# Kernel optimization log

Measured on AMD Instinct MI355X. Metric: run time of the kernel, lower is better.

The kernel has to match this reference:

```python
import jax, jax.numpy as jnp
import numpy as np

N = 100000
IN_DIM = 256
OUT_DIM = 256
E = 3200000
SLOPE = 0.2


def setup_inputs() -> dict:
    key = jax.random.key(0)
    ks = jax.random.split(key, 14)
    xav = lambda k, shape: jax.random.normal(k, shape, jnp.float32) * np.sqrt(2.0 / sum(shape))
    inp = {
        "H": jax.random.normal(ks[0], (N, IN_DIM), jnp.float32),
        "W0": xav(ks[1], (IN_DIM, OUT_DIM)),
        "W1": xav(ks[2], (IN_DIM, OUT_DIM)),
        "W2": xav(ks[3], (IN_DIM, OUT_DIM)),
        "a0": xav(ks[4], (2 * OUT_DIM,)),
        "a1": xav(ks[5], (2 * OUT_DIM,)),
        "a2": xav(ks[6], (2 * OUT_DIM,)),
        "bias": jnp.zeros((OUT_DIM,), jnp.float32),
    }
    for i, r in enumerate(["0", "1", "2"]):
        inp["row" + r] = jax.random.randint(ks[7 + 2 * i], (E,), 0, N, jnp.int32)
        inp["col" + r] = jax.random.randint(ks[8 + 2 * i], (E,), 0, N, jnp.int32)
    return inp


def _gat_type(H, W, a, row, col):
    # Wh: [N, out_dim]
    Wh = H @ W
    # attention logits per edge: leaky_relu(a_dst . Wh[row] + a_src . Wh[col])
    s_dst = Wh @ a[:OUT_DIM]   # [N]
    s_src = Wh @ a[OUT_DIM:]   # [N]
    e = jax.nn.leaky_relu(s_dst[row] + s_src[col], SLOPE)  # [E]
    # segment softmax over destination node (row)
    e_max = jax.ops.segment_max(e, row, num_segments=N)    # [N]
    e_shifted = jnp.exp(e - e_max[row])
    e_sum = jax.ops.segment_sum(e_shifted, row, num_segments=N)
    alpha = e_shifted / jnp.maximum(e_sum[row], 1e-12)     # [E]
    # weighted aggregation of source features into destinations
    return jax.ops.segment_sum(alpha[:, None] * Wh[col], row, num_segments=N)


def reference(H, row0, col0, row1, col1, row2, col2, W0, W1, W2, a0, a1, a2, bias):
    out = _gat_type(H, W0, a0, row0, col0)
    out = out + _gat_type(H, W1, a1, row1, col1)
    out = out + _gat_type(H, W2, a2, row2, col2)
    return out + bias
```

## Files before the change

### kernel.cpp

```cpp
#include <hip/hip_runtime.h>
#include <cstdint>
#include <cstddef>

#define DIM 256
#define SLOPE 0.2f
#define BSHIFT 8
#define SLOTS 9216
#define TILE 4096

typedef __attribute__((ext_vector_type(8))) short short8;
typedef __attribute__((ext_vector_type(4))) float f32x4;

__device__ __forceinline__ unsigned short f2bf(float f) {
  unsigned u = __float_as_uint(f);
  u += 0x7fffu + ((u >> 16) & 1u);
  return (unsigned short)(u >> 16);
}
__device__ __forceinline__ float bf2f(unsigned short h) {
  return __uint_as_float(((unsigned)h) << 16);
}


__device__ __forceinline__ void bin_edges_body(
    int bx, int ty, int* hist, int* curs, const int* __restrict__ rr,
    const int* __restrict__ cc, int* __restrict__ bcnt, unsigned* __restrict__ pairs,
    int E, int NB) {
  const int t = threadIdx.x;
  const int base = bx * TILE;
  for (int i = t; i < NB; i += 256) hist[i] = 0;
  __syncthreads();
  int rows[TILE / 256];
#pragma unroll
  for (int i = 0; i < TILE / 256; ++i) {
    int e = base + t + i * 256;
    int r = (e < E) ? rr[e] : -1;
    rows[i] = r;
    if (r >= 0) atomicAdd(&hist[r >> BSHIFT], 1);
  }
  __syncthreads();
  for (int b = t; b < NB; b += 256) {
    int h = hist[b];
    int off = h ? atomicAdd(&bcnt[ty * NB + b], h) : 0;
    curs[b] = b * SLOTS + off;
  }
  __syncthreads();
  unsigned* pt = pairs + (size_t)ty * NB * SLOTS;
#pragma unroll
  for (int i = 0; i < TILE / 256; ++i) {
    int e = base + t + i * 256;
    if (e >= E) continue;
    int r = rows[i];
    int b = r >> BSHIFT;
    int pos = atomicAdd(&curs[b], 1);
    if (pos - b * SLOTS < SLOTS)
      pt[pos] = ((unsigned)(r & 255) << 17) | (unsigned)cc[e];
  }
}

__device__ __forceinline__ void bsort_body(
    int b, int ty, char* smem, const int* __restrict__ bcnt,
    unsigned* __restrict__ pairs, int* __restrict__ rp, int* __restrict__ deg,
    int N, int NB) {
  int* hist = (int*)smem;
  int* excl = hist + 256;
  int* curs = excl + 256;
  unsigned* stage = (unsigned*)(curs + 256);
  const int t = threadIdx.x;
  int cnt = bcnt[ty * NB + b];
  if (cnt > SLOTS) cnt = SLOTS;
  unsigned* pb = pairs + (size_t)ty * NB * SLOTS + (size_t)b * SLOTS;
  hist[t] = 0;
  __syncthreads();
  for (int i = t; i < cnt; i += 256) atomicAdd(&hist[pb[i] >> 17], 1);
  __syncthreads();
  int v = hist[t];
  excl[t] = v;
  __syncthreads();
  for (int off = 1; off < 256; off <<= 1) {
    int u = (t >= off) ? excl[t - off] : 0;
    __syncthreads();
    excl[t] += u;
    __syncthreads();
  }
  int ex = excl[t] - v;
  curs[t] = ex;
  int r = (b << BSHIFT) + t;
  if (r < N) {
    rp[(size_t)ty * N + r] = b * SLOTS + ex;
    deg[(size_t)ty * N + r] = v;
  }
  __syncthreads();
  for (int i = t; i < cnt; i += 256) {
    unsigned p = pb[i];
    int pos = atomicAdd(&curs[p >> 17], 1);
    stage[pos] = p;
  }
  __syncthreads();
  for (int i = t; i < cnt; i += 256) pb[i] = stage[i];
}

__device__ __forceinline__ void gemm3_body(
    int bx, char* smem, const float* __restrict__ H, const unsigned short* __restrict__ Wt,
    const float* __restrict__ a0, const float* __restrict__ a1,
    const float* __restrict__ a2, unsigned short* __restrict__ Whb,
    float* __restrict__ s_dst, float* __restrict__ s_src, int N, size_t wstride) {
  unsigned short(*Hs)[264] = (unsigned short(*)[264])smem;
  unsigned short(*Os)[4][264] = (unsigned short(*)[4][264])(smem + 128 * 264 * 2);
  const int t = threadIdx.x;
  const int r0 = bx * 128;
#pragma unroll
  for (int i = 0; i < 32; ++i) {
    int idx = t + i * 256;
    int row = idx >> 6;
    int c4 = idx & 63;
    int r = r0 + row;
    float4 h = (r < N) ? *(const float4*)&H[(size_t)r * DIM + c4 * 4]
                       : make_float4(0.f, 0.f, 0.f, 0.f);
    unsigned lo = (unsigned)f2bf(h.x) | ((unsigned)f2bf(h.y) << 16);
    unsigned hi = (unsigned)f2bf(h.z) | ((unsigned)f2bf(h.w) << 16);
    *(uint2*)&Hs[row][c4 * 4] = make_uint2(lo, hi);
  }
  __syncthreads();
  const int wave = t >> 6, lane = t & 63;
  const int q = lane >> 4, m = lane & 15;
  const int rowbase = wave * 32;
  short8 Af0[8], Af1[8];
#pragma unroll
  for (int k0 = 0; k0 < 8; ++k0) {
    Af0[k0] = *(const short8*)&Hs[rowbase + m][k0 * 32 + q * 8];
    Af1[k0] = *(const short8*)&Hs[rowbase + 16 + m][k0 * 32 + q * 8];
  }
  const float* aptr[3] = {a0, a1, a2};
  for (int ty = 0; ty < 3; ++ty) {
    const unsigned short* Wtt = Wt + (size_t)ty * DIM * DIM;
    const float* a = aptr[ty];
    f32x4 acc0[16], acc1[16];
#pragma unroll
    for (int j = 0; j < 16; ++j) {
      acc0[j] = (f32x4){0.f, 0.f, 0.f, 0.f};
      acc1[j] = (f32x4){0.f, 0.f, 0.f, 0.f};
    }
#pragma unroll
    for (int k0 = 0; k0 < 8; ++k0) {
#pragma unroll
      for (int j = 0; j < 16; ++j) {
        short8 Bf = *(const short8*)&Wtt[(size_t)(j * 16 + m) * DIM + k0 * 32 + q * 8];
        acc0[j] = __builtin_amdgcn_mfma_f32_16x16x32_bf16(Af0[k0], Bf, acc0[j], 0, 0, 0);
        acc1[j] = __builtin_amdgcn_mfma_f32_16x16x32_bf16(Af1[k0], Bf, acc1[j], 0, 0, 0);
      }
    }
    float pd0[4] = {0, 0, 0, 0}, ps0[4] = {0, 0, 0, 0};
    float pd1[4] = {0, 0, 0, 0}, ps1[4] = {0, 0, 0, 0};
#pragma unroll
    for (int j = 0; j < 16; ++j) {
      int col = j * 16 + m;
      float ad = a[col], as = a[DIM + col];
#pragma unroll
      for (int reg = 0; reg < 4; ++reg) {
        float v0 = acc0[j][reg], v1 = acc1[j][reg];
        pd0[reg] += v0 * ad;
        ps0[reg] += v0 * as;
        pd1[reg] += v1 * ad;
        ps1[reg] += v1 * as;
      }
    }
#pragma unroll
    for (int off = 8; off >= 1; off >>= 1) {
#pragma unroll
      for (int reg = 0; reg < 4; ++reg) {
        pd0[reg] += __shfl_down(pd0[reg], off);
        ps0[reg] += __shfl_down(ps0[reg], off);
        pd1[reg] += __shfl_down(pd1[reg], off);
        ps1[reg] += __shfl_down(ps1[reg], off);
      }
    }
    if (m == 0) {
#pragma unroll
      for (int reg = 0; reg < 4; ++reg) {
        int ra = r0 + rowbase + q * 4 + reg;
        int rb = ra + 16;
        if (ra < N) {
          s_dst[(size_t)ty * N + ra] = pd0[reg];
          s_src[(size_t)ty * N + ra] = ps0[reg];
        }
        if (rb < N) {
          s_dst[(size_t)ty * N + rb] = pd1[reg];
          s_src[(size_t)ty * N + rb] = ps1[reg];
        }
      }
    }
    unsigned short* wout = Whb + (size_t)ty * wstride;
#pragma unroll
    for (int g = 0; g < 2; ++g) {
#pragma unroll
      for (int p = 0; p < 4; ++p) {
        if (q == p) {
#pragma unroll
          for (int j = 0; j < 16; ++j)
#pragma unroll
            for (int reg = 0; reg < 4; ++reg)
              Os[wave][reg][j * 16 + m] = f2bf(g ? acc1[j][reg] : acc0[j][reg]);
        }
#pragma unroll
        for (int rr = 0; rr < 4; ++rr) {
          int r = r0 + rowbase + g * 16 + p * 4 + rr;
          if (r < N)
            *(uint2*)&wout[(size_t)r * DIM + lane * 4] =
                *(const uint2*)&Os[wave][rr][lane * 4];
        }
      }
    }
  }
}


__global__ __launch_bounds__(256) void prep_kernel(
    const float* __restrict__ W0, const float* __restrict__ W1,
    const float* __restrict__ W2, unsigned short* __restrict__ Wt,
    const int* __restrict__ r0, const int* __restrict__ r1, const int* __restrict__ r2,
    const int* __restrict__ c0, const int* __restrict__ c1, const int* __restrict__ c2,
    int* __restrict__ bcnt, unsigned* __restrict__ pairs, int E, int NB, int eb) {
  __shared__ int smem[1024];
  const int bx = blockIdx.x;
  if (bx < 768) {
    int ty = bx >> 8, k = bx & 255, n = threadIdx.x;
    const float* W = ty == 0 ? W0 : (ty == 1 ? W1 : W2);
    Wt[((size_t)ty * DIM + n) * DIM + k] = f2bf(W[k * DIM + n]);
    return;
  }
  int e2 = bx - 768;
  int ty = e2 / eb, bxx = e2 % eb;
  const int* rr = ty == 0 ? r0 : (ty == 1 ? r1 : r2);
  const int* cc = ty == 0 ? c0 : (ty == 1 ? c1 : c2);
  bin_edges_body(bxx, ty, smem, smem + 512, rr, cc, bcnt, pairs, E, NB);
}

__global__ __launch_bounds__(256, 2) void compute_kernel(
    const float* __restrict__ H, const unsigned short* __restrict__ Wt,
    const float* __restrict__ a0, const float* __restrict__ a1,
    const float* __restrict__ a2, unsigned short* __restrict__ Whb,
    float* __restrict__ s_dst, float* __restrict__ s_src, int N, size_t wstride,
    const int* __restrict__ bcnt, unsigned* __restrict__ pairs,
    int* __restrict__ rp, int* __restrict__ deg, int NB, int gemm_blocks) {
  __shared__ __align__(16) char smem[76032];
  const int bx = blockIdx.x;
  if (bx < gemm_blocks) {
    gemm3_body(bx, smem, H, Wt, a0, a1, a2, Whb, s_dst, s_src, N, wstride);
  } else {
    int e = bx - gemm_blocks;
    bsort_body(e % NB, e / NB, smem, bcnt, pairs, rp, deg, N, NB);
  }
}

__global__ __launch_bounds__(256) void bucket_sort_kernel(
    const int* __restrict__ bcnt, unsigned* __restrict__ pairs,
    int* __restrict__ rp, int* __restrict__ deg, int N, int NB) {
  __shared__ __align__(16) char smem[39936];
  bsort_body(blockIdx.x, blockIdx.y, smem, bcnt, pairs, rp, deg, N, NB);
}

__global__ __launch_bounds__(256, 2) void gemm_scores_kernel(
    const float* __restrict__ H, const unsigned short* __restrict__ Wt,
    const float* __restrict__ a, unsigned short* __restrict__ Whb,
    float* __restrict__ s_dst, float* __restrict__ s_src, int N) {
  __shared__ unsigned short Hs[64][264];
  __shared__ unsigned short Os[4][16][264];
  const int t = threadIdx.x;
  const int r0 = blockIdx.x * 64;
#pragma unroll
  for (int i = 0; i < 16; ++i) {
    int idx = t + i * 256;
    int row = idx >> 6;
    int c4 = idx & 63;
    int r = r0 + row;
    float4 h = (r < N) ? *(const float4*)&H[(size_t)r * DIM + c4 * 4]
                       : make_float4(0.f, 0.f, 0.f, 0.f);
    unsigned lo = (unsigned)f2bf(h.x) | ((unsigned)f2bf(h.y) << 16);
    unsigned hi = (unsigned)f2bf(h.z) | ((unsigned)f2bf(h.w) << 16);
    *(uint2*)&Hs[row][c4 * 4] = make_uint2(lo, hi);
  }
  __syncthreads();
  const int wave = t >> 6, lane = t & 63;
  const int q = lane >> 4, m = lane & 15;
  const int rowbase = wave * 16;
  short8 Af[8];
#pragma unroll
  for (int k0 = 0; k0 < 8; ++k0)
    Af[k0] = *(const short8*)&Hs[rowbase + m][k0 * 32 + q * 8];
  f32x4 acc[16];
#pragma unroll
  for (int j = 0; j < 16; ++j) acc[j] = (f32x4){0.f, 0.f, 0.f, 0.f};
#pragma unroll
  for (int k0 = 0; k0 < 8; ++k0) {
#pragma unroll
    for (int j = 0; j < 16; ++j) {
      short8 Bf = *(const short8*)&Wt[(size_t)(j * 16 + m) * DIM + k0 * 32 + q * 8];
      acc[j] = __builtin_amdgcn_mfma_f32_16x16x32_bf16(Af[k0], Bf, acc[j], 0, 0, 0);
    }
  }
  float pd[4] = {0, 0, 0, 0}, ps[4] = {0, 0, 0, 0};
#pragma unroll
  for (int j = 0; j < 16; ++j) {
    int col = j * 16 + m;
    float ad = a[col], as = a[DIM + col];
#pragma unroll
    for (int reg = 0; reg < 4; ++reg) {
      float v = acc[j][reg];
      pd[reg] += v * ad;
      ps[reg] += v * as;
      Os[wave][q * 4 + reg][col] = f2bf(v);
    }
  }
#pragma unroll
  for (int off = 8; off >= 1; off >>= 1) {
#pragma unroll
    for (int reg = 0; reg < 4; ++reg) {
      pd[reg] += __shfl_down(pd[reg], off);
      ps[reg] += __shfl_down(ps[reg], off);
    }
  }
  if (m == 0) {
#pragma unroll
    for (int reg = 0; reg < 4; ++reg) {
      int r = r0 + rowbase + q * 4 + reg;
      if (r < N) {
        s_dst[r] = pd[reg];
        s_src[r] = ps[reg];
      }
    }
  }
  __syncthreads();
#pragma unroll
  for (int row = 0; row < 16; ++row) {
    int r = r0 + rowbase + row;
    if (r < N)
      *(uint2*)&Whb[(size_t)r * DIM + lane * 4] = *(const uint2*)&Os[wave][row][lane * 4];
  }
}

__global__ __launch_bounds__(256) void gat_fused_kernel(
    const int* __restrict__ rp, const int* __restrict__ deg,
    const unsigned* __restrict__ pairs,
    const float* __restrict__ s_dst, const float* __restrict__ s_src,
    const unsigned short* __restrict__ Whb,
    const float* __restrict__ bias, float* __restrict__ out, int N, int NB,
    size_t wstride) {
  __shared__ uint2 ebuf[4][64];
  int n = (int)((blockIdx.x * (unsigned)blockDim.x + threadIdx.x) >> 6);
  if (n >= N) return;
  const int wid = (threadIdx.x >> 6);
  const int lane = threadIdx.x & 63;
  float4 total = {0.f, 0.f, 0.f, 0.f};
  for (int t = 0; t < 3; ++t) {
    int beg = rp[(size_t)t * N + n], d = deg[(size_t)t * N + n];
    if (d == 0) continue;
    int end = beg + d;
    const unsigned* pcol = pairs + (size_t)t * NB * SLOTS;
    const float* ss = s_src + (size_t)t * N;
    float sd = s_dst[(size_t)t * N + n];
    const unsigned short* wbase = Whb + (size_t)t * wstride + lane * 4;
    float mx = -__builtin_inff();
    for (int p = beg + lane; p < end; p += 64) {
      float v = sd + ss[pcol[p] & 0x1FFFFu];
      v = v > 0.f ? v : SLOPE * v;
      mx = fmaxf(mx, v);
    }
#pragma unroll
    for (int off = 32; off >= 1; off >>= 1) mx = fmaxf(mx, __shfl_down(mx, off));
    mx = __shfl(mx, 0);
    float4 acc = {0.f, 0.f, 0.f, 0.f};
    float psum = 0.f;
    for (int base = beg; base < end; base += 64) {
      int myp = base + lane;
      int cnt = end - base;
      if (cnt > 64) cnt = 64;
      unsigned myc = 0;
      float mype = 0.f;
      if (myp < end) {
        myc = pcol[myp] & 0x1FFFFu;
        float v = sd + ss[myc];
        v = v > 0.f ? v : SLOPE * v;
        mype = __expf(v - mx);
      }
      psum += mype;
      ebuf[wid][lane] = make_uint2(myc, __float_as_uint(mype));
#pragma unroll 8
      for (int j = 0; j < cnt; ++j) {
        uint2 cp = ebuf[wid][j];
        float pe = __uint_as_float(cp.y);
        ushort4 w = *(const ushort4*)&wbase[(size_t)cp.x * DIM];
        acc.x += pe * bf2f(w.x);
        acc.y += pe * bf2f(w.y);
        acc.z += pe * bf2f(w.z);
        acc.w += pe * bf2f(w.w);
      }
    }
#pragma unroll
    for (int off = 32; off >= 1; off >>= 1) psum += __shfl_down(psum, off);
    psum = __shfl(psum, 0);
    float inv = 1.f / fmaxf(psum, 1e-12f);
    total.x += acc.x * inv;
    total.y += acc.y * inv;
    total.z += acc.z * inv;
    total.w += acc.w * inv;
  }
  float4 cur = ((const float4*)bias)[lane];
  cur.x += total.x;
  cur.y += total.y;
  cur.z += total.z;
  cur.w += total.w;
  *((float4*)(out + (size_t)n * DIM) + lane) = cur;
}

__global__ __launch_bounds__(256) void gat_node_kernel(
    const int* __restrict__ rp, const int* __restrict__ deg,
    const unsigned* __restrict__ pcol,
    const float* __restrict__ s_dst, const float* __restrict__ s_src,
    const unsigned short* __restrict__ Whb,
    const float* __restrict__ bias, float* __restrict__ out, int N, int first) {
  __shared__ uint2 ebuf[4][64];
  int n = (int)((blockIdx.x * (unsigned)blockDim.x + threadIdx.x) >> 6);
  if (n >= N) return;
  const int wid = (threadIdx.x >> 6);
  const int lane = threadIdx.x & 63;
  int beg = rp[n], d = deg[n], end = beg + d;
  if (!first && d == 0) return;
  float sd = s_dst[n];
  float mx = -__builtin_inff();
  for (int p = beg + lane; p < end; p += 64) {
    float v = sd + s_src[pcol[p] & 0x1FFFFu];
    v = v > 0.f ? v : SLOPE * v;
    mx = fmaxf(mx, v);
  }
#pragma unroll
  for (int off = 32; off >= 1; off >>= 1) mx = fmaxf(mx, __shfl_down(mx, off));
  mx = __shfl(mx, 0);
  const unsigned short* wbase = Whb + lane * 4;
  float4 acc = {0.f, 0.f, 0.f, 0.f};
  float psum = 0.f;
  for (int base = beg; base < end; base += 64) {
    int myp = base + lane;
    int cnt = end - base;
    if (cnt > 64) cnt = 64;
    unsigned myc = 0;
    float mype = 0.f;
    if (myp < end) {
      myc = pcol[myp] & 0x1FFFFu;
      float v = sd + s_src[myc];
      v = v > 0.f ? v : SLOPE * v;
      mype = __expf(v - mx);
    }
    psum += mype;
    ebuf[wid][lane] = make_uint2(myc, __float_as_uint(mype));
#pragma unroll 8
    for (int j = 0; j < cnt; ++j) {
      uint2 cp = ebuf[wid][j];
      float pe = __uint_as_float(cp.y);
      ushort4 w = *(const ushort4*)&wbase[(size_t)cp.x * DIM];
      acc.x += pe * bf2f(w.x);
      acc.y += pe * bf2f(w.y);
      acc.z += pe * bf2f(w.z);
      acc.w += pe * bf2f(w.w);
    }
  }
#pragma unroll
  for (int off = 32; off >= 1; off >>= 1) psum += __shfl_down(psum, off);
  psum = __shfl(psum, 0);
  float inv = 1.f / fmaxf(psum, 1e-12f);
  float4* o = (float4*)(out + (size_t)n * DIM) + lane;
  float4 cur = first ? ((const float4*)bias)[lane] : *o;
  cur.x += acc.x * inv;
  cur.y += acc.y * inv;
  cur.z += acc.z * inv;
  cur.w += acc.w * inv;
  *o = cur;
}

static inline size_t align256(size_t x) { return (x + 255) & ~(size_t)255; }

extern "C" void kernel_launch(void* const* d_in, const int* in_sizes, int n_in,
                              void* d_out, int out_size, void* d_ws, size_t ws_size,
                              hipStream_t stream) {
  const float* H = (const float*)d_in[0];
  const float* W[3] = {(const float*)d_in[1], (const float*)d_in[2], (const float*)d_in[3]};
  const float* a[3] = {(const float*)d_in[4], (const float*)d_in[5], (const float*)d_in[6]};
  const float* bias = (const float*)d_in[7];
  const int* row[3] = {(const int*)d_in[8], (const int*)d_in[10], (const int*)d_in[12]};
  const int* col[3] = {(const int*)d_in[9], (const int*)d_in[11], (const int*)d_in[13]};
  const int N = in_sizes[0] / DIM;
  const int E = in_sizes[8];
  const int NB = (N + 255) >> BSHIFT;
  float* out = (float*)d_out;

  char* ws = (char*)d_ws;
  size_t off = 0;
  unsigned short* Wt = (unsigned short*)(ws + off);
  off = align256(off + (size_t)3 * DIM * DIM * sizeof(unsigned short));
  float* s_dst = (float*)(ws + off);
  off = align256(off + (size_t)3 * N * sizeof(float));
  float* s_src = (float*)(ws + off);
  off = align256(off + (size_t)3 * N * sizeof(float));
  int* bcnt = (int*)(ws + off);
  off = align256(off + (size_t)3 * NB * sizeof(int));
  int* rp = (int*)(ws + off);
  off = align256(off + (size_t)3 * N * sizeof(int));
  int* deg = (int*)(ws + off);
  off = align256(off + (size_t)3 * N * sizeof(int));
  unsigned* pairs = (unsigned*)(ws + off);
  off = align256(off + (size_t)3 * NB * SLOTS * sizeof(unsigned));
  unsigned short* Whb = (unsigned short*)(ws + off);
  const size_t whb_bytes = align256((size_t)N * DIM * sizeof(unsigned short));
  const size_t wstride = whb_bytes / sizeof(unsigned short);
  const int fused = (ws_size >= off + 3 * whb_bytes) ? 1 : 0;

  const int eb = (E + TILE - 1) / TILE;
  hipMemsetAsync(bcnt, 0, (size_t)3 * NB * sizeof(int), stream);
  prep_kernel<<<768 + 3 * eb, 256, 0, stream>>>(W[0], W[1], W[2], Wt, row[0], row[1], row[2],
                                                col[0], col[1], col[2], bcnt, pairs, E, NB, eb);

  const int gat_blocks = (N * 64 + 255) / 256;
  if (fused) {
    const int gemm_blocks = (N + 127) / 128;
    compute_kernel<<<gemm_blocks + 3 * NB, 256, 0, stream>>>(
        H, Wt, a[0], a[1], a[2], Whb, s_dst, s_src, N, wstride, bcnt, pairs, rp, deg, NB,
        gemm_blocks);
    gat_fused_kernel<<<gat_blocks, 256, 0, stream>>>(rp, deg, pairs, s_dst, s_src, Whb, bias,
                                                     out, N, NB, wstride);
  } else {
    bucket_sort_kernel<<<dim3(NB, 3), 256, 0, stream>>>(bcnt, pairs, rp, deg, N, NB);
    for (int t = 0; t < 3; ++t) {
      gemm_scores_kernel<<<(N + 63) / 64, 256, 0, stream>>>(H, Wt + (size_t)t * DIM * DIM,
                                                            a[t], Whb, s_dst + (size_t)t * N,
                                                            s_src + (size_t)t * N, N);
      gat_node_kernel<<<gat_blocks, 256, 0, stream>>>(
          rp + (size_t)t * N, deg + (size_t)t * N, pairs + (size_t)t * NB * SLOTS,
          s_dst + (size_t)t * N, s_src + (size_t)t * N, Whb, bias, out, N, t == 0 ? 1 : 0);
    }
  }
  (void)n_in;
  (void)out_size;
  (void)ws_size;
}
```

Baseline: 1.387 ms.

## Overlap type-0 aggregation with type-1/2 GEMMs in an interleaved kernel

The fused compute kernel now runs only the type-0 GEMM alongside the bucket sort. A new kernel interleaves blocks that run a leaner GEMM for types 1 and 2 with blocks that aggregate type-0 edges and write bias plus the type-0 result. A final kernel then adds the type-1 and type-2 aggregations into the output with a read-modify-write. This is meant to hide GEMM compute behind memory-bound gather work, at the cost of an extra pass over the output and relying on blocks being scheduled in index order.

```diff
diff --git a/kernel.cpp b/kernel.cpp
--- a/kernel.cpp
+++ b/kernel.cpp
@@ -103,7 +103,8 @@
     int bx, char* smem, const float* __restrict__ H, const unsigned short* __restrict__ Wt,
     const float* __restrict__ a0, const float* __restrict__ a1,
     const float* __restrict__ a2, unsigned short* __restrict__ Whb,
-    float* __restrict__ s_dst, float* __restrict__ s_src, int N, size_t wstride) {
+    float* __restrict__ s_dst, float* __restrict__ s_src, int N, size_t wstride,
+    int tycount) {
   unsigned short(*Hs)[264] = (unsigned short(*)[264])smem;
   unsigned short(*Os)[4][264] = (unsigned short(*)[4][264])(smem + 128 * 264 * 2);
   const int t = threadIdx.x;
@@ -131,7 +132,7 @@
     Af1[k0] = *(const short8*)&Hs[rowbase + 16 + m][k0 * 32 + q * 8];
   }
   const float* aptr[3] = {a0, a1, a2};
-  for (int ty = 0; ty < 3; ++ty) {
+  for (int ty = 0; ty < tycount; ++ty) {
     const unsigned short* Wtt = Wt + (size_t)ty * DIM * DIM;
     const float* a = aptr[ty];
     f32x4 acc0[16], acc1[16];
@@ -208,6 +209,98 @@
             *(uint2*)&wout[(size_t)r * DIM + lane * 4] =
                 *(const uint2*)&Os[wave][rr][lane * 4];
         }
+      }
+    }
+  }
+}
+
+__device__ __forceinline__ void gemm1_lean_body(
+    int bx, int ty, char* smem, const float* __restrict__ H,
+    const unsigned short* __restrict__ Wt, const float* __restrict__ a,
+    unsigned short* __restrict__ Whb, float* __restrict__ s_dst,
+    float* __restrict__ s_src, int N, size_t wstride) {
+  unsigned short(*Os)[4][264] = (unsigned short(*)[4][264])smem;
+  const int t = threadIdx.x;
+  const int r0 = bx * 64;
+  const int wave = t >> 6, lane = t & 63;
+  const int q = lane >> 4, m = lane & 15;
+  const int rowbase = wave * 16;
+  const int myrow = r0 + rowbase + m;
+  short8 Af[8];
+#pragma unroll
+  for (int k0 = 0; k0 < 8; ++k0) {
+    short8 v = (short8){0, 0, 0, 0, 0, 0, 0, 0};
+    if (myrow < N) {
+      const float* hp = &H[(size_t)myrow * DIM + k0 * 32 + q * 8];
+      float4 x = *(const float4*)hp;
+      float4 y = *(const float4*)(hp + 4);
+      v[0] = (short)f2bf(x.x); v[1] = (short)f2bf(x.y);
+      v[2] = (short)f2bf(x.z); v[3] = (short)f2bf(x.w);
+      v[4] = (short)f2bf(y.x); v[5] = (short)f2bf(y.y);
+      v[6] = (short)f2bf(y.z); v[7] = (short)f2bf(y.w);
+    }
+    Af[k0] = v;
+  }
+  const unsigned short* Wtt = Wt + (size_t)ty * DIM * DIM;
+  unsigned short* wout = Whb + (size_t)ty * wstride;
+  float pd[4] = {0, 0, 0, 0}, ps[4] = {0, 0, 0, 0};
+  for (int jh = 0; jh < 2; ++jh) {
+    f32x4 acc[8];
+#pragma unroll
+    for (int j = 0; j < 8; ++j) acc[j] = (f32x4){0.f, 0.f, 0.f, 0.f};
+#pragma unroll
+    for (int k0 = 0; k0 < 8; ++k0) {
+#pragma unroll
+      for (int j = 0; j < 8; ++j) {
+        int col16 = jh * 8 + j;
+        short8 Bf = *(const short8*)&Wtt[(size_t)(col16 * 16 + m) * DIM + k0 * 32 + q * 8];
+        acc[j] = __builtin_amdgcn_mfma_f32_16x16x32_bf16(Af[k0], Bf, acc[j], 0, 0, 0);
+      }
+    }
+#pragma unroll
+    for (int j = 0; j < 8; ++j) {
+      int col = (jh * 8 + j) * 16 + m;
+      float ad = a[col], as = a[DIM + col];
+#pragma unroll
+      for (int reg = 0; reg < 4; ++reg) {
+        float v = acc[j][reg];
+        pd[reg] += v * ad;
+        ps[reg] += v * as;
+      }
+    }
+#pragma unroll
+    for (int p = 0; p < 4; ++p) {
+      if (q == p) {
+#pragma unroll
+        for (int j = 0; j < 8; ++j)
+#pragma unroll
+          for (int reg = 0; reg < 4; ++reg)
+            Os[wave][reg][(jh * 8 + j) * 16 + m] = f2bf(acc[j][reg]);
+      }
+#pragma unroll
+      for (int rr = 0; rr < 4; ++rr) {
+        int r = r0 + rowbase + p * 4 + rr;
+        if (r < N)
+          *(unsigned*)&wout[(size_t)r * DIM + jh * 128 + lane * 2] =
+              *(const unsigned*)&Os[wave][rr][jh * 128 + lane * 2];
+      }
+    }
+  }
+#pragma unroll
+  for (int off = 8; off >= 1; off >>= 1) {
+#pragma unroll
+    for (int reg = 0; reg < 4; ++reg) {
+      pd[reg] += __shfl_down(pd[reg], off);
+      ps[reg] += __shfl_down(ps[reg], off);
+    }
+  }
+  if (m == 0) {
+#pragma unroll
+    for (int reg = 0; reg < 4; ++reg) {
+      int r = r0 + rowbase + q * 4 + reg;
+      if (r < N) {
+        s_dst[(size_t)ty * N + r] = pd[reg];
+        s_src[(size_t)ty * N + r] = ps[reg];
       }
     }
   }
@@ -241,109 +334,96 @@
     const float* __restrict__ a2, unsigned short* __restrict__ Whb,
     float* __restrict__ s_dst, float* __restrict__ s_src, int N, size_t wstride,
     const int* __restrict__ bcnt, unsigned* __restrict__ pairs,
-    int* __restrict__ rp, int* __restrict__ deg, int NB, int gemm_blocks) {
+    int* __restrict__ rp, int* __restrict__ deg, int NB, int gemm_blocks,
+    int tycount) {
   __shared__ __align__(16) char smem[76032];
   const int bx = blockIdx.x;
   if (bx < gemm_blocks) {
-    gemm3_body(bx, smem, H, Wt, a0, a1, a2, Whb, s_dst, s_src, N, wstride);
+    gemm3_body(bx, smem, H, Wt, a0, a1, a2, Whb, s_dst, s_src, N, wstride, tycount);
   } else {
     int e = bx - gemm_blocks;
     bsort_body(e % NB, e / NB, smem, bcnt, pairs, rp, deg, N, NB);
   }
 }
 
-__global__ __launch_bounds__(256) void bucket_sort_kernel(
-    const int* __restrict__ bcnt, unsigned* __restrict__ pairs,
-    int* __restrict__ rp, int* __restrict__ deg, int N, int NB) {
-  __shared__ __align__(16) char smem[39936];
-  bsort_body(blockIdx.x, blockIdx.y, smem, bcnt, pairs, rp, deg, N, NB);
-}
-
-__global__ __launch_bounds__(256, 2) void gemm_scores_kernel(
+__global__ __launch_bounds__(256, 4) void gat0_gemm_kernel(
     const float* __restrict__ H, const unsigned short* __restrict__ Wt,
-    const float* __restrict__ a, unsigned short* __restrict__ Whb,
-    float* __restrict__ s_dst, float* __restrict__ s_src, int N) {
-  __shared__ unsigned short Hs[64][264];
-  __shared__ unsigned short Os[4][16][264];
-  const int t = threadIdx.x;
-  const int r0 = blockIdx.x * 64;
-#pragma unroll
-  for (int i = 0; i < 16; ++i) {
-    int idx = t + i * 256;
-    int row = idx >> 6;
-    int c4 = idx & 63;
-    int r = r0 + row;
-    float4 h = (r < N) ? *(const float4*)&H[(size_t)r * DIM + c4 * 4]
-                       : make_float4(0.f, 0.f, 0.f, 0.f);
-    unsigned lo = (unsigned)f2bf(h.x) | ((unsigned)f2bf(h.y) << 16);
-    unsigned hi = (unsigned)f2bf(h.z) | ((unsigned)f2bf(h.w) << 16);
-    *(uint2*)&Hs[row][c4 * 4] = make_uint2(lo, hi);
-  }
-  __syncthreads();
-  const int wave = t >> 6, lane = t & 63;
-  const int q = lane >> 4, m = lane & 15;
-  const int rowbase = wave * 16;
-  short8 Af[8];
-#pragma unroll
-  for (int k0 = 0; k0 < 8; ++k0)
-    Af[k0] = *(const short8*)&Hs[rowbase + m][k0 * 32 + q * 8];
-  f32x4 acc[16];
-#pragma unroll
-  for (int j = 0; j < 16; ++j) acc[j] = (f32x4){0.f, 0.f, 0.f, 0.f};
-#pragma unroll
-  for (int k0 = 0; k0 < 8; ++k0) {
-#pragma unroll
-    for (int j = 0; j < 16; ++j) {
-      short8 Bf = *(const short8*)&Wt[(size_t)(j * 16 + m) * DIM + k0 * 32 + q * 8];
-      acc[j] = __builtin_amdgcn_mfma_f32_16x16x32_bf16(Af[k0], Bf, acc[j], 0, 0, 0);
-    }
-  }
-  float pd[4] = {0, 0, 0, 0}, ps[4] = {0, 0, 0, 0};
-#pragma unroll
-  for (int j = 0; j < 16; ++j) {
-    int col = j * 16 + m;
-    float ad = a[col], as = a[DIM + col];
-#pragma unroll
-    for (int reg = 0; reg < 4; ++reg) {
-      float v = acc[j][reg];
-      pd[reg] += v * ad;
-      ps[reg] += v * as;
-      Os[wave][q * 4 + reg][col] = f2bf(v);
-    }
-  }
-#pragma unroll
-  for (int off = 8; off >= 1; off >>= 1) {
-#pragma unroll
-    for (int reg = 0; reg < 4; ++reg) {
-      pd[reg] += __shfl_down(pd[reg], off);
-      ps[reg] += __shfl_down(ps[reg], off);
-    }
-  }
-  if (m == 0) {
-#pragma unroll
-    for (int reg = 0; reg < 4; ++reg) {
-      int r = r0 + rowbase + q * 4 + reg;
-      if (r < N) {
-        s_dst[r] = pd[reg];
-        s_src[r] = ps[reg];
-      }
-    }
-  }
-  __syncthreads();
-#pragma unroll
-  for (int row = 0; row < 16; ++row) {
-    int r = r0 + rowbase + row;
-    if (r < N)
-      *(uint2*)&Whb[(size_t)r * DIM + lane * 4] = *(const uint2*)&Os[wave][row][lane * 4];
-  }
-}
-
-__global__ __launch_bounds__(256) void gat_fused_kernel(
+    const float* __restrict__ a1, const float* __restrict__ a2,
+    unsigned short* __restrict__ Whb, float* __restrict__ s_dst,
+    float* __restrict__ s_src, const int* __restrict__ rp, const int* __restrict__ deg,
+    const unsigned* __restrict__ pairs, const float* __restrict__ bias,
+    float* __restrict__ out, int N, size_t wstride, int gemmB, int R) {
+  __shared__ __align__(16) char smem[8448];
+  const int bx = blockIdx.x;
+  int g = bx / R;
+  if (bx - g * R == 0 && g < gemmB) {
+    int ty = 1 + (g & 1);
+    gemm1_lean_body(g >> 1, ty, smem, H, Wt, (ty == 1 ? a1 : a2), Whb, s_dst, s_src, N,
+                    wstride);
+    return;
+  }
+  int gidx = (g < gemmB) ? (bx - g - 1) : (bx - gemmB);
+  int n = gidx * 4 + (threadIdx.x >> 6);
+  if (n >= N) return;
+  uint2(*ebuf)[64] = (uint2(*)[64])smem;
+  const int wid = threadIdx.x >> 6;
+  const int lane = threadIdx.x & 63;
+  int beg = rp[n], d = deg[n], end = beg + d;
+  float sd = s_dst[n];
+  float mx = -__builtin_inff();
+  for (int p = beg + lane; p < end; p += 64) {
+    float v = sd + s_src[pairs[p] & 0x1FFFFu];
+    v = v > 0.f ? v : SLOPE * v;
+    mx = fmaxf(mx, v);
+  }
+#pragma unroll
+  for (int off = 32; off >= 1; off >>= 1) mx = fmaxf(mx, __shfl_down(mx, off));
+  mx = __shfl(mx, 0);
+  const unsigned short* wbase = Whb + lane * 4;
+  float4 acc = {0.f, 0.f, 0.f, 0.f};
+  float psum = 0.f;
+  for (int base = beg; base < end; base += 64) {
+    int myp = base + lane;
+    int cnt = end - base;
+    if (cnt > 64) cnt = 64;
+    unsigned myc = 0;
+    float mype = 0.f;
+    if (myp < end) {
+      myc = pairs[myp] & 0x1FFFFu;
+      float v = sd + s_src[myc];
+      v = v > 0.f ? v : SLOPE * v;
+      mype = __expf(v - mx);
+    }
+    psum += mype;
+    ebuf[wid][lane] = make_uint2(myc, __float_as_uint(mype));
+#pragma unroll 8
+    for (int j = 0; j < cnt; ++j) {
+      uint2 cp = ebuf[wid][j];
+      float pe = __uint_as_float(cp.y);
+      ushort4 w = *(const ushort4*)&wbase[(size_t)cp.x * DIM];
+      acc.x += pe * bf2f(w.x);
+      acc.y += pe * bf2f(w.y);
+      acc.z += pe * bf2f(w.z);
+      acc.w += pe * bf2f(w.w);
+    }
+  }
+#pragma unroll
+  for (int off = 32; off >= 1; off >>= 1) psum += __shfl_down(psum, off);
+  psum = __shfl(psum, 0);
+  float inv = 1.f / fmaxf(psum, 1e-12f);
+  float4 cur = ((const float4*)bias)[lane];
+  cur.x += acc.x * inv;
+  cur.y += acc.y * inv;
+  cur.z += acc.z * inv;
+  cur.w += acc.w * inv;
+  *((float4*)(out + (size_t)n * DIM) + lane) = cur;
+}
+
+__global__ __launch_bounds__(256) void gat12_kernel(
     const int* __restrict__ rp, const int* __restrict__ deg,
     const unsigned* __restrict__ pairs,
     const float* __restrict__ s_dst, const float* __restrict__ s_src,
-    const unsigned short* __restrict__ Whb,
-    const float* __restrict__ bias, float* __restrict__ out, int N, int NB,
+    const unsigned short* __restrict__ Whb, float* __restrict__ out, int N, int NB,
     size_t wstride) {
   __shared__ uint2 ebuf[4][64];
   int n = (int)((blockIdx.x * (unsigned)blockDim.x + threadIdx.x) >> 6);
@@ -351,9 +431,11 @@
   const int wid = (threadIdx.x >> 6);
   const int lane = threadIdx.x & 63;
   float4 total = {0.f, 0.f, 0.f, 0.f};
-  for (int t = 0; t < 3; ++t) {
+  int any = 0;
+  for (int t = 1; t < 3; ++t) {
     int beg = rp[(size_t)t * N + n], d = deg[(size_t)t * N + n];
     if (d == 0) continue;
+    any = 1;
     int end = beg + d;
     const unsigned* pcol = pairs + (size_t)t * NB * SLOTS;
     const float* ss = s_src + (size_t)t * N;
@@ -404,12 +486,101 @@
     total.z += acc.z * inv;
     total.w += acc.w * inv;
   }
-  float4 cur = ((const float4*)bias)[lane];
+  if (!any) return;
+  float4* o = (float4*)(out + (size_t)n * DIM) + lane;
+  float4 cur = *o;
   cur.x += total.x;
   cur.y += total.y;
   cur.z += total.z;
   cur.w += total.w;
-  *((float4*)(out + (size_t)n * DIM) + lane) = cur;
+  *o = cur;
+}
+
+
+__global__ __launch_bounds__(256) void bucket_sort_kernel(
+    const int* __restrict__ bcnt, unsigned* __restrict__ pairs,
+    int* __restrict__ rp, int* __restrict__ deg, int N, int NB) {
+  __shared__ __align__(16) char smem[39936];
+  bsort_body(blockIdx.x, blockIdx.y, smem, bcnt, pairs, rp, deg, N, NB);
+}
+
+__global__ __launch_bounds__(256, 2) void gemm_scores_kernel(
+    const float* __restrict__ H, const unsigned short* __restrict__ Wt,
+    const float* __restrict__ a, unsigned short* __restrict__ Whb,
+    float* __restrict__ s_dst, float* __restrict__ s_src, int N) {
+  __shared__ unsigned short Hs[64][264];
+  __shared__ unsigned short Os[4][16][264];
+  const int t = threadIdx.x;
+  const int r0 = blockIdx.x * 64;
+#pragma unroll
+  for (int i = 0; i < 16; ++i) {
+    int idx = t + i * 256;
+    int row = idx >> 6;
+    int c4 = idx & 63;
+    int r = r0 + row;
+    float4 h = (r < N) ? *(const float4*)&H[(size_t)r * DIM + c4 * 4]
+                       : make_float4(0.f, 0.f, 0.f, 0.f);
+    unsigned lo = (unsigned)f2bf(h.x) | ((unsigned)f2bf(h.y) << 16);
+    unsigned hi = (unsigned)f2bf(h.z) | ((unsigned)f2bf(h.w) << 16);
+    *(uint2*)&Hs[row][c4 * 4] = make_uint2(lo, hi);
+  }
+  __syncthreads();
+  const int wave = t >> 6, lane = t & 63;
+  const int q = lane >> 4, m = lane & 15;
+  const int rowbase = wave * 16;
+  short8 Af[8];
+#pragma unroll
+  for (int k0 = 0; k0 < 8; ++k0)
+    Af[k0] = *(const short8*)&Hs[rowbase + m][k0 * 32 + q * 8];
+  f32x4 acc[16];
+#pragma unroll
+  for (int j = 0; j < 16; ++j) acc[j] = (f32x4){0.f, 0.f, 0.f, 0.f};
+#pragma unroll
+  for (int k0 = 0; k0 < 8; ++k0) {
+#pragma unroll
+    for (int j = 0; j < 16; ++j) {
+      short8 Bf = *(const short8*)&Wt[(size_t)(j * 16 + m) * DIM + k0 * 32 + q * 8];
+      acc[j] = __builtin_amdgcn_mfma_f32_16x16x32_bf16(Af[k0], Bf, acc[j], 0, 0, 0);
+    }
+  }
+  float pd[4] = {0, 0, 0, 0}, ps[4] = {0, 0, 0, 0};
+#pragma unroll
+  for (int j = 0; j < 16; ++j) {
+    int col = j * 16 + m;
+    float ad = a[col], as = a[DIM + col];
+#pragma unroll
+    for (int reg = 0; reg < 4; ++reg) {
+      float v = acc[j][reg];
+      pd[reg] += v * ad;
+      ps[reg] += v * as;
+      Os[wave][q * 4 + reg][col] = f2bf(v);
+    }
+  }
+#pragma unroll
+  for (int off = 8; off >= 1; off >>= 1) {
+#pragma unroll
+    for (int reg = 0; reg < 4; ++reg) {
+      pd[reg] += __shfl_down(pd[reg], off);
+      ps[reg] += __shfl_down(ps[reg], off);
+    }
+  }
+  if (m == 0) {
+#pragma unroll
+    for (int reg = 0; reg < 4; ++reg) {
+      int r = r0 + rowbase + q * 4 + reg;
+      if (r < N) {
+        s_dst[r] = pd[reg];
+        s_src[r] = ps[reg];
+      }
+    }
+  }
+  __syncthreads();
+#pragma unroll
+  for (int row = 0; row < 16; ++row) {
+    int r = r0 + rowbase + row;
+    if (r < N)
+      *(uint2*)&Whb[(size_t)r * DIM + lane * 4] = *(const uint2*)&Os[wave][row][lane * 4];
+  }
 }
 
 __global__ __launch_bounds__(256) void gat_node_kernel(
@@ -520,12 +691,19 @@
 
   const int gat_blocks = (N * 64 + 255) / 256;
   if (fused) {
-    const int gemm_blocks = (N + 127) / 128;
-    compute_kernel<<<gemm_blocks + 3 * NB, 256, 0, stream>>>(
+    const int nb128 = (N + 127) / 128;
+    compute_kernel<<<nb128 + 3 * NB, 256, 0, stream>>>(
         H, Wt, a[0], a[1], a[2], Whb, s_dst, s_src, N, wstride, bcnt, pairs, rp, deg, NB,
-        gemm_blocks);
-    gat_fused_kernel<<<gat_blocks, 256, 0, stream>>>(rp, deg, pairs, s_dst, s_src, Whb, bias,
-                                                     out, N, NB, wstride);
+        nb128, 1 );
+    const int nb64 = (N + 63) / 64;
+    const int gemmB = 2 * nb64;
+    int R = gat_blocks / gemmB + 1;
+    if (R < 2) R = 2;
+    const int gridC = gat_blocks + gemmB + R;
+    gat0_gemm_kernel<<<gridC, 256, 0, stream>>>(H, Wt, a[1], a[2], Whb, s_dst, s_src, rp, deg,
+                                                pairs, bias, out, N, wstride, gemmB, R);
+    gat12_kernel<<<gat_blocks, 256, 0, stream>>>(rp, deg, pairs, s_dst, s_src, Whb, out, N,
+                                                 NB, wstride);
   } else {
     bucket_sort_kernel<<<dim3(NB, 3), 256, 0, stream>>>(bcnt, pairs, rp, deg, N, NB);
     for (int t = 0; t < 3; ++t) {
```

Measured after the change: 2.938 ms. +111.8%, slower.
